# Kernel tuning notes

Measured on AMD Instinct MI355X. Metric: run time of the kernel, lower is better.

Reference implementation:

```python
import jax, jax.numpy as jnp
import numpy as np

B, S, SC, E, H = 2, 2048, 2048, 1024, 16
D = E // H
EPS = 1e-6


def _layernorm(x, g, b):
    m = jnp.mean(x, axis=-1, keepdims=True)
    v = jnp.mean((x - m) ** 2, axis=-1, keepdims=True)
    return (x - m) / jnp.sqrt(v + EPS) * g + b


def _mha(xk, xv, xq, Wk, Wv, Wq, Wo, bo, masked):
    # per-head projections, vectorized over the head axis: [B,Sx,E] x [H,E,D] -> [B,H,Sx,D]
    K = jnp.einsum('bse,hed->bhsd', xk, Wk)
    V = jnp.einsum('bse,hed->bhsd', xv, Wv)
    Q = jnp.einsum('bqe,hed->bhqd', xq, Wq)
    scores = jnp.einsum('bhqd,bhkd->bhqk', Q, K)  # [B,H,Sq,Sk]
    sk = xk.shape[1]
    if masked:
        causal = jnp.triu(jnp.ones((xq.shape[1], sk), dtype=bool), k=1)
        scores = jnp.where(causal, -jnp.inf, scores)
    att = jax.nn.softmax(scores / jnp.sqrt(jnp.asarray(sk, scores.dtype)), axis=-1)
    out = jnp.einsum('bhqk,bhkd->bhqd', att, V)
    out = out.transpose(0, 2, 1, 3).reshape(out.shape[0], out.shape[2], -1)  # concat heads -> [B,Sq,E]
    return jax.nn.relu(out @ Wo + bo)  # Dense(emb_sz, relu) output projection


def setup_inputs():
    key = jax.random.key(0)
    ks = jax.random.split(key, 16)
    w = lambda k, shape: jax.random.normal(k, shape, jnp.float32) * 0.02
    return {
        'inputs': jax.random.normal(ks[0], (B, S, E), jnp.float32),
        'context_seq': jax.random.normal(ks[1], (B, SC, E), jnp.float32),
        'Wk1': w(ks[2], (H, E, D)), 'Wv1': w(ks[3], (H, E, D)), 'Wq1': w(ks[4], (H, E, D)),
        'Wo1': w(ks[5], (E, E)), 'bo1': jnp.zeros((E,), jnp.float32),
        'Wk2': w(ks[6], (H, E, D)), 'Wv2': w(ks[7], (H, E, D)), 'Wq2': w(ks[8], (H, E, D)),
        'Wo2': w(ks[9], (E, E)), 'bo2': jnp.zeros((E,), jnp.float32),
        'Wf': w(ks[10], (E, E)), 'bf': jnp.zeros((E,), jnp.float32),
        'g1': jnp.ones((E,), jnp.float32), 'b1': jnp.zeros((E,), jnp.float32),
        'g2': jnp.ones((E,), jnp.float32), 'b2': jnp.zeros((E,), jnp.float32),
        'g3': jnp.ones((E,), jnp.float32), 'b3': jnp.zeros((E,), jnp.float32),
    }


def reference(inputs, context_seq, Wk1, Wv1, Wq1, Wo1, bo1,
              Wk2, Wv2, Wq2, Wo2, bo2, Wf, bf,
              g1, b1, g2, b2, g3, b3):
    # masked multi-head self-attention + residual + LN1 (dropout is identity at inference)
    a = _mha(inputs, inputs, inputs, Wk1, Wv1, Wq1, Wo1, bo1, masked=True)
    a = _layernorm(inputs + a, g1, b1)
    # unmasked cross-attention: K/V from context, Q from previous output
    c = _mha(context_seq, context_seq, a, Wk2, Wv2, Wq2, Wo2, bo2, masked=False)
    c = _layernorm(c + c, g2, b2)  # faithful to source: residual adds output to itself
    # FFN (single Dense(emb_sz, relu)) + residual + LN3
    f = jax.nn.relu(c @ Wf + bf)
    return _layernorm(c + f, g3, b3)
```

## Files before the change

### kernel.cpp

```cpp
#include <hip/hip_runtime.h>
#include <stdint.h>
#include <stddef.h>

typedef __bf16 bf16;
typedef __bf16 bf16x8 __attribute__((ext_vector_type(8)));
typedef __bf16 bf16x4 __attribute__((ext_vector_type(4)));
typedef float  f32x4  __attribute__((ext_vector_type(4)));
typedef uint32_t u32x4 __attribute__((ext_vector_type(4)));

#define MFMA(a, b, c) __builtin_amdgcn_mfma_f32_16x16x32_bf16((a), (b), (c), 0, 0, 0)
#define SWZE(row, chunk) (((row) << 6) + ((((chunk) ^ ((row) & 7))) << 3))

static __device__ __forceinline__ void gload_lds16(const void* g, void* l) {
  __builtin_amdgcn_global_load_lds((const __attribute__((address_space(1))) void*)g,
                                   (__attribute__((address_space(3))) void*)l,
                                   16, 0, 0);
}
static __device__ __forceinline__ void waitvm0() {
  asm volatile("s_waitcnt vmcnt(0)" ::: "memory");
}
static __device__ __forceinline__ float expq(float x) {
  float r;
  asm("v_exp_f32 %0, %1" : "=v"(r) : "v"(x));
  return r;
}
static __device__ __forceinline__ float rcpq(float x) {
  float r;
  asm("v_rcp_f32 %0, %1" : "=v"(r) : "v"(x));
  return r;
}
static __device__ __forceinline__ uint32_t cvtpk_bf16(float lo, float hi) {
  uint32_t r;
  asm("v_cvt_pk_bf16_f32 %0, %1, %2" : "=v"(r) : "v"(lo), "v"(hi));
  return r;
}
static __device__ __forceinline__ int xcd_swz(int orig, int nwg) {
  return (orig & 7) * (nwg >> 3) + (orig >> 3);
}
static __device__ __forceinline__ int vperm_store(int s) {
  return (s & ~31) | (((s >> 3) & 1) << 4) | (((s >> 2) & 1) << 3) |
         (((s >> 4) & 1) << 2) | (s & 3);
}

__global__ __launch_bounds__(256) void prep_k(
    const float* __restrict__ inp, const float* __restrict__ ctx,
    bf16* __restrict__ XB, bf16* __restrict__ CB,
    const float* __restrict__ Wq1, const float* __restrict__ Wk1,
    const float* __restrict__ Wv1, const float* __restrict__ Wq2,
    const float* __restrict__ Wk2, const float* __restrict__ Wv2,
    bf16* __restrict__ WQKV1, bf16* __restrict__ WQ2, bf16* __restrict__ WKV2,
    const float* __restrict__ Wo1, const float* __restrict__ Wo2,
    const float* __restrict__ Wf,
    bf16* __restrict__ WO1, bf16* __restrict__ WO2, bf16* __restrict__ WFt) {
  const int tid = threadIdx.x;
  int bx = blockIdx.x;
  if (bx < 8192) {
    const float* s = bx < 4096 ? inp : ctx;
    bf16* d = bx < 4096 ? XB : CB;
    size_t idx = (size_t)(bx & 4095) * 256 + tid;
    float4 v = *(const float4*)(s + idx * 4);
    bf16x4 o;
    o[0] = (bf16)v.x; o[1] = (bf16)v.y; o[2] = (bf16)v.z; o[3] = (bf16)v.w;
    *(bf16x4*)(d + idx * 4) = o;
    return;
  }
  bx -= 8192;
  __shared__ float T[64][65];
  if (bx < 1536) {
    const int wi = bx >> 8, sub = bx & 255;
    const float* src = (wi == 0) ? Wq1 : (wi == 1) ? Wk1 : (wi == 2) ? Wv1
                     : (wi == 3) ? Wq2 : (wi == 4) ? Wk2 : Wv2;
    bf16* dst = (wi == 0) ? WQKV1 : (wi == 1) ? WQKV1 + 1048576
              : (wi == 2) ? WQKV1 + 2097152 : (wi == 3) ? WQ2
              : (wi == 4) ? WKV2 : WKV2 + 1048576;
    const int e0 = (sub & 15) * 64, h = sub >> 4;
    const int er = tid >> 4, dof = (tid & 15) * 4;
#pragma unroll
    for (int i = 0; i < 4; ++i) {
      int e = i * 16 + er;
      float4 v = *(const float4*)(src + ((size_t)h * 1024 + e0 + e) * 64 + dof);
      T[e][dof] = v.x; T[e][dof + 1] = v.y; T[e][dof + 2] = v.z; T[e][dof + 3] = v.w;
    }
    __syncthreads();
    const int dr = tid >> 3, eo = (tid & 7) * 8;
#pragma unroll
    for (int i = 0; i < 2; ++i) {
      int d = i * 32 + dr;
      bf16x8 ov;
#pragma unroll
      for (int j = 0; j < 8; ++j) ov[j] = (bf16)T[eo + j][d];
      *(bf16x8*)(dst + ((size_t)h * 64 + d) * 1024 + e0 + eo) = ov;
    }
    return;
  }
  bx -= 1536;
  {
    const int wi = bx >> 8, sub = bx & 255;
    const float* src = (wi == 0) ? Wo1 : (wi == 1) ? Wo2 : Wf;
    bf16* dst = (wi == 0) ? WO1 : (wi == 1) ? WO2 : WFt;
    const int k0 = (sub & 15) * 64, n0 = (sub >> 4) * 64;
    const int kr = tid >> 4, no = (tid & 15) * 4;
#pragma unroll
    for (int i = 0; i < 4; ++i) {
      int k = i * 16 + kr;
      float4 v = *(const float4*)(src + (size_t)(k0 + k) * 1024 + n0 + no);
      T[k][no] = v.x; T[k][no + 1] = v.y; T[k][no + 2] = v.z; T[k][no + 3] = v.w;
    }
    __syncthreads();
    const int nr = tid >> 3, ko = (tid & 7) * 8;
#pragma unroll
    for (int i = 0; i < 2; ++i) {
      int n = i * 32 + nr;
      bf16x8 ov;
#pragma unroll
      for (int j = 0; j < 8; ++j) ov[j] = (bf16)T[ko + j][n];
      *(bf16x8*)(dst + (size_t)(n0 + n) * 1024 + k0 + ko) = ov;
    }
  }
}

template <int EPI>
static __device__ __forceinline__ void gemm_body(
    const bf16* __restrict__ A, const bf16* __restrict__ Bt,
    bf16* __restrict__ Cb, float* __restrict__ Cf,
    const float* __restrict__ bias, const float* __restrict__ resid,
    int N, int K, float mul, int m0, int n0, bf16* As, bf16* Bs,
    bf16* __restrict__ Vt, int colV) {
  const int tid = threadIdx.x;
  const int l = tid & 63, w = tid >> 6;
  const int l15 = l & 15, g4 = l >> 4;
  const int wr = w >> 1, wc = w & 1;
  f32x4 acc[4][4] = {};
  const int crow = tid >> 3;
  const int cko = (tid & 7) * 8;
  for (int k0 = 0; k0 < K; k0 += 64) {
#pragma unroll
    for (int i = 0; i < 4; ++i) {
      int row = i * 32 + crow;
      gload_lds16(A + (size_t)(m0 + row) * K + (k0 + cko), (char*)As + (i * 256 + tid) * 16);
      gload_lds16(Bt + (size_t)(n0 + row) * K + (k0 + cko), (char*)Bs + (i * 256 + tid) * 16);
    }
    __syncthreads();
#pragma unroll
    for (int kk = 0; kk < 2; ++kk) {
      bf16x8 af[4], bfr[4];
#pragma unroll
      for (int x = 0; x < 4; ++x) {
        af[x]  = *(const bf16x8*)&As[(wr * 64 + x * 16 + l15) * 64 + kk * 32 + g4 * 8];
        bfr[x] = *(const bf16x8*)&Bs[(wc * 64 + x * 16 + l15) * 64 + kk * 32 + g4 * 8];
      }
      __builtin_amdgcn_s_setprio(1);
#pragma unroll
      for (int mf = 0; mf < 4; ++mf)
#pragma unroll
        for (int nf = 0; nf < 4; ++nf)
          acc[mf][nf] = MFMA(af[mf], bfr[nf], acc[mf][nf]);
      __builtin_amdgcn_s_setprio(0);
    }
    __syncthreads();
  }
  if (EPI == 2 && n0 >= colV) {
#pragma unroll
    for (int mf = 0; mf < 4; ++mf)
#pragma unroll
      for (int nf = 0; nf < 4; ++nf) {
        int colrel = n0 + wc * 64 + nf * 16 + l15 - colV;
        int h = colrel >> 6, d = colrel & 63;
        int row = m0 + wr * 64 + mf * 16 + g4 * 4;
        int b = row >> 11, s = row & 2047;
        bf16x4 pv;
#pragma unroll
        for (int r = 0; r < 4; ++r) pv[r] = (bf16)acc[mf][nf][r];
        *(bf16x4*)(Vt + (((size_t)(b * 16 + h) * 64 + d) * 2048 + vperm_store(s))) = pv;
      }
    return;
  }
#pragma unroll
  for (int mf = 0; mf < 4; ++mf)
#pragma unroll
    for (int nf = 0; nf < 4; ++nf)
#pragma unroll
      for (int r = 0; r < 4; ++r) {
        int row = m0 + wr * 64 + mf * 16 + g4 * 4 + r;
        int col = n0 + wc * 64 + nf * 16 + l15;
        size_t idx = (size_t)row * N + col;
        float v = acc[mf][nf][r];
        if (EPI == 1) {
          v = mul * fmaxf(v + bias[col], 0.f);
          if (resid) v += resid[idx];
          Cf[idx] = v;
        } else {
          Cb[idx] = (bf16)v;
        }
      }
}

__global__ __launch_bounds__(256) void gemm_qkv_k(
    const bf16* __restrict__ A, const bf16* __restrict__ Bt,
    bf16* __restrict__ Cb, bf16* __restrict__ Vt, int N, int K, int colV) {
  __shared__ __align__(16) bf16 As[128 * 64];
  __shared__ __align__(16) bf16 Bs[128 * 64];
  int swz = xcd_swz(blockIdx.y * gridDim.x + blockIdx.x, gridDim.x * gridDim.y);
  int bx = swz % gridDim.x, by = swz / gridDim.x;
  gemm_body<2>(A, Bt, Cb, nullptr, nullptr, nullptr, N, K, 1.f,
               by * 128, bx * 128, As, Bs, Vt, colV);
}

__global__ __launch_bounds__(256) void gemm_bt2_k(
    const bf16* __restrict__ A0, const bf16* __restrict__ Bt0, bf16* __restrict__ C0,
    const bf16* __restrict__ A1, const bf16* __restrict__ Bt1, bf16* __restrict__ C1,
    bf16* __restrict__ Vt, int K) {
  __shared__ __align__(16) bf16 As[128 * 64];
  __shared__ __align__(16) bf16 Bs[128 * 64];
  int swz = xcd_swz(blockIdx.y * gridDim.x + blockIdx.x, gridDim.x * gridDim.y);
  int bx = swz % gridDim.x, by = swz / gridDim.x;
  if (bx < 8)
    gemm_body<0>(A0, Bt0, C0, nullptr, nullptr, nullptr, 1024, K, 1.f,
                 by * 128, bx * 128, As, Bs, nullptr, 1 << 30);
  else
    gemm_body<2>(A1, Bt1, C1, nullptr, nullptr, nullptr, 2048, K, 1.f,
                 by * 128, (bx - 8) * 128, As, Bs, Vt, 1024);
}

template <int EPI>
__global__ __launch_bounds__(512) void gemm64_k(
    const bf16* __restrict__ A, const bf16* __restrict__ Bt,
    bf16* __restrict__ Cb, float* __restrict__ Cf,
    const float* __restrict__ bias, const float* __restrict__ resid,
    int N, int K, float mul) {
  __shared__ __align__(16) bf16 As[64 * 64];
  __shared__ __align__(16) bf16 Bs[128 * 64];
  const int tid = threadIdx.x;
  const int l = tid & 63, w = tid >> 6;
  const int l15 = l & 15, g4 = l >> 4;
  const int wr = w >> 2, wc = w & 3;
  int swz = xcd_swz(blockIdx.y * gridDim.x + blockIdx.x, gridDim.x * gridDim.y);
  const int m0 = (swz / gridDim.x) * 64, n0 = (swz % gridDim.x) * 128;
  f32x4 acc[2][2] = {};
  const int crow = tid >> 3, cko = (tid & 7) * 8;
  for (int k0 = 0; k0 < K; k0 += 64) {
    gload_lds16(A + (size_t)(m0 + crow) * K + (k0 + cko), (char*)As + tid * 16);
#pragma unroll
    for (int i = 0; i < 2; ++i) {
      int row = i * 64 + crow;
      gload_lds16(Bt + (size_t)(n0 + row) * K + (k0 + cko), (char*)Bs + (i * 512 + tid) * 16);
    }
    __syncthreads();
#pragma unroll
    for (int kk = 0; kk < 2; ++kk) {
      bf16x8 af[2], bfr[2];
#pragma unroll
      for (int x = 0; x < 2; ++x) {
        af[x]  = *(const bf16x8*)&As[(wr * 32 + x * 16 + l15) * 64 + kk * 32 + g4 * 8];
        bfr[x] = *(const bf16x8*)&Bs[(wc * 32 + x * 16 + l15) * 64 + kk * 32 + g4 * 8];
      }
      __builtin_amdgcn_s_setprio(1);
#pragma unroll
      for (int mf = 0; mf < 2; ++mf)
#pragma unroll
        for (int nf = 0; nf < 2; ++nf)
          acc[mf][nf] = MFMA(af[mf], bfr[nf], acc[mf][nf]);
      __builtin_amdgcn_s_setprio(0);
    }
    __syncthreads();
  }
#pragma unroll
  for (int mf = 0; mf < 2; ++mf)
#pragma unroll
    for (int nf = 0; nf < 2; ++nf)
#pragma unroll
      for (int r = 0; r < 4; ++r) {
        int row = m0 + wr * 32 + mf * 16 + g4 * 4 + r;
        int col = n0 + wc * 32 + nf * 16 + l15;
        size_t idx = (size_t)row * N + col;
        float v = acc[mf][nf][r];
        if (EPI == 0) {
          Cb[idx] = (bf16)v;
        } else {
          v = mul * fmaxf(v + bias[col], 0.f);
          if (resid) v += resid[idx];
          Cf[idx] = v;
        }
      }
}

template <int CAUSAL>
__global__ __launch_bounds__(256) void attn_k(
    const bf16* __restrict__ Q, int ldq, size_t sBq,
    const bf16* __restrict__ Kp, int ldk, size_t sBk,
    const bf16* __restrict__ Vt,
    bf16* __restrict__ O, int ldo, size_t sBo,
    int Sk) {
  __shared__ __align__(16) char smem[32768];
  bf16* const KsBase = (bf16*)smem;
  bf16* const VsBase = (bf16*)(smem + 16384);
  const int tid = threadIdx.x;
  const int l = tid & 63, w = tid >> 6;
  const int l15 = l & 15, g4 = l >> 4;
  const int qh = w >> 1, kh = w & 1;
  const int orig = blockIdx.y * gridDim.x + blockIdx.x;
  int qt, bh;
  if (CAUSAL) {
    const int slot = orig >> 8, s = orig & 255;
    const int pb = s & 31;
    qt = (slot & 1) ? (31 - pb) : pb;
    bh = (s >> 5) * 4 + slot;
  } else {
    const int swz = xcd_swz(orig, gridDim.x * gridDim.y);
    qt = swz % gridDim.x;
    bh = swz / gridDim.x;
  }
  const int b = bh >> 4, h = bh & 15;
  const int nT = Sk >> 6;
  const int total = CAUSAL ? (qt + 1) : nT;
  const int q0b = qt * 64;
  const bf16* Qb = Q + (size_t)b * sBq + h * 64;
  const bf16* Kb = Kp + (size_t)b * sBk + h * 64;
  const bf16* Vb = Vt + ((size_t)bh * 64) * Sk;
  bf16* Ob = O + (size_t)b * sBo + h * 64;
  const float sc2 = rsqrtf((float)Sk) * 1.442695040888963f;

  bf16x8 qf[2][2];
#pragma unroll
  for (int qg = 0; qg < 2; ++qg)
#pragma unroll
    for (int kk = 0; kk < 2; ++kk) {
      bf16x8 t8 = *(const bf16x8*)(Qb + (size_t)(q0b + qh * 32 + qg * 16 + l15) * ldq +
                                   kk * 32 + g4 * 8);
#pragma unroll
      for (int j = 0; j < 8; ++j) t8[j] = (bf16)((float)t8[j] * sc2);
      qf[qg][kk] = t8;
    }

  bf16x8 onesb;
#pragma unroll
  for (int j = 0; j < 8; ++j) onesb[j] = (bf16)1.0f;

  f32x4 o[2][4] = {};
  f32x4 ol[2] = {};

  const int srow = tid >> 3, sj = tid & 7;
  auto stage = [&](int ch, int bufi) {
#pragma unroll
    for (int ii = 0; ii < 2; ++ii) {
      int row = ii * 32 + srow;
      int je = ((sj ^ (row & 7)) << 3);
      gload_lds16(Kb + (size_t)(ch * 64 + row) * ldk + je,
                  (char*)(KsBase + bufi * 4096) + (ii * 256 + tid) * 16);
      gload_lds16(Vb + (size_t)row * Sk + ch * 64 + je,
                  (char*)(VsBase + bufi * 4096) + (ii * 256 + tid) * 16);
    }
  };

  stage(0, 0);
  waitvm0();
  __builtin_amdgcn_s_barrier();

  int cur = 0;

  for (int i = 0; i < total; ++i) {
    if (i + 1 < total) stage(i + 1, cur ^ 1);

    const int k0 = i * 64;
    const bf16* ks = KsBase + cur * 4096;
    const bf16* vs = VsBase + cur * 4096;

    f32x4 s[2][2] = {};
    __builtin_amdgcn_s_setprio(1);
#pragma unroll
    for (int ksub = 0; ksub < 2; ++ksub)
#pragma unroll
      for (int kk = 0; kk < 2; ++kk) {
        bf16x8 kf = *(const bf16x8*)&ks[SWZE(kh * 32 + ksub * 16 + l15, kk * 4 + g4)];
        s[ksub][0] = MFMA(kf, qf[0][kk], s[ksub][0]);
        s[ksub][1] = MFMA(kf, qf[1][kk], s[ksub][1]);
      }
    __builtin_amdgcn_s_setprio(0);

    if (CAUSAL && i == total - 1) {
#pragma unroll
      for (int ksub = 0; ksub < 2; ++ksub)
#pragma unroll
        for (int qg = 0; qg < 2; ++qg)
#pragma unroll
          for (int r = 0; r < 4; ++r)
            if ((k0 + kh * 32 + ksub * 16 + g4 * 4 + r) > (q0b + qh * 32 + qg * 16 + l15))
              s[ksub][qg][r] = -3e38f;
    }

#pragma unroll
    for (int ksub = 0; ksub < 2; ++ksub)
#pragma unroll
      for (int qg = 0; qg < 2; ++qg) {
        s[ksub][qg][0] = expq(s[ksub][qg][0]);
        s[ksub][qg][1] = expq(s[ksub][qg][1]);
        s[ksub][qg][2] = expq(s[ksub][qg][2]);
        s[ksub][qg][3] = expq(s[ksub][qg][3]);
      }

    bf16x8 vf[4];
#pragma unroll
    for (int nf2 = 0; nf2 < 4; ++nf2)
      vf[nf2] = *(const bf16x8*)&vs[SWZE(nf2 * 16 + l15, kh * 4 + g4)];

    __builtin_amdgcn_s_setprio(1);
#pragma unroll
    for (int qg = 0; qg < 2; ++qg) {
      u32x4 td;
      td[0] = cvtpk_bf16(s[0][qg][0], s[0][qg][1]);
      td[1] = cvtpk_bf16(s[0][qg][2], s[0][qg][3]);
      td[2] = cvtpk_bf16(s[1][qg][0], s[1][qg][1]);
      td[3] = cvtpk_bf16(s[1][qg][2], s[1][qg][3]);
      bf16x8 pa = __builtin_bit_cast(bf16x8, td);
#pragma unroll
      for (int nf2 = 0; nf2 < 4; ++nf2)
        o[qg][nf2] = MFMA(pa, vf[nf2], o[qg][nf2]);
      ol[qg] = MFMA(pa, onesb, ol[qg]);
    }
    __builtin_amdgcn_s_setprio(0);

    waitvm0();
    __builtin_amdgcn_s_barrier();
    cur ^= 1;
  }

  {
    float* sc = (float*)smem;
    float* my = sc + (size_t)(qh * 64 + l) * 41;
    if (kh == 1) {
#pragma unroll
      for (int qg = 0; qg < 2; ++qg) {
#pragma unroll
        for (int nf2 = 0; nf2 < 4; ++nf2)
#pragma unroll
          for (int r = 0; r < 4; ++r) my[(qg * 4 + nf2) * 4 + r] = o[qg][nf2][r];
#pragma unroll
        for (int r = 0; r < 4; ++r) my[32 + qg * 4 + r] = ol[qg][r];
      }
    }
    __syncthreads();
    if (kh == 0) {
#pragma unroll
      for (int qg = 0; qg < 2; ++qg) {
        f32x4 lsum;
#pragma unroll
        for (int r = 0; r < 4; ++r) lsum[r] = ol[qg][r] + my[32 + qg * 4 + r];
        float inv[4];
#pragma unroll
        for (int r = 0; r < 4; ++r) inv[r] = rcpq(lsum[r]);
#pragma unroll
        for (int nf2 = 0; nf2 < 4; ++nf2)
#pragma unroll
          for (int r = 0; r < 4; ++r) {
            float v = (o[qg][nf2][r] + my[(qg * 4 + nf2) * 4 + r]) * inv[r];
            Ob[(size_t)(q0b + qh * 32 + qg * 16 + g4 * 4 + r) * ldo + nf2 * 16 + l15] = (bf16)v;
          }
      }
    }
  }
}

__global__ __launch_bounds__(256) void ln_k(const float* __restrict__ X,
                                            const float* __restrict__ g,
                                            const float* __restrict__ bta,
                                            bf16* __restrict__ outb,
                                            float* __restrict__ outf) {
  const int tid = threadIdx.x;
  const size_t row = blockIdx.x;
  const float* x = X + row * 1024;
  float4 v = *(const float4*)(x + tid * 4);
  float sum = v.x + v.y + v.z + v.w;
  float sq = v.x * v.x + v.y * v.y + v.z * v.z + v.w * v.w;
#pragma unroll
  for (int m = 1; m < 64; m <<= 1) {
    sum += __shfl_xor(sum, m);
    sq += __shfl_xor(sq, m);
  }
  __shared__ float s1[4], s2[4];
  int w = tid >> 6;
  if ((tid & 63) == 0) { s1[w] = sum; s2[w] = sq; }
  __syncthreads();
  sum = s1[0] + s1[1] + s1[2] + s1[3];
  sq = s2[0] + s2[1] + s2[2] + s2[3];
  float mean = sum * (1.f / 1024.f);
  float var = sq * (1.f / 1024.f) - mean * mean;
  float inv = rsqrtf(var + 1e-6f);
  float4 gv = *(const float4*)(g + tid * 4);
  float4 bv = *(const float4*)(bta + tid * 4);
  float y0 = (v.x - mean) * inv * gv.x + bv.x;
  float y1 = (v.y - mean) * inv * gv.y + bv.y;
  float y2 = (v.z - mean) * inv * gv.z + bv.z;
  float y3 = (v.w - mean) * inv * gv.w + bv.w;
  if (outb) {
    bf16x4 ob;
    ob[0] = (bf16)y0; ob[1] = (bf16)y1; ob[2] = (bf16)y2; ob[3] = (bf16)y3;
    *(bf16x4*)(outb + row * 1024 + tid * 4) = ob;
  }
  if (outf) {
    float4 of;
    of.x = y0; of.y = y1; of.z = y2; of.w = y3;
    *(float4*)(outf + row * 1024 + tid * 4) = of;
  }
}

extern "C" void kernel_launch(void* const* d_in, const int* in_sizes, int n_in,
                              void* d_out, int out_size, void* d_ws, size_t ws_size,
                              hipStream_t stream) {
  (void)in_sizes; (void)n_in; (void)out_size; (void)ws_size;
  const float* inp = (const float*)d_in[0];
  const float* ctx = (const float*)d_in[1];
  const float* Wk1 = (const float*)d_in[2];
  const float* Wv1 = (const float*)d_in[3];
  const float* Wq1 = (const float*)d_in[4];
  const float* Wo1 = (const float*)d_in[5];
  const float* bo1 = (const float*)d_in[6];
  const float* Wk2 = (const float*)d_in[7];
  const float* Wv2 = (const float*)d_in[8];
  const float* Wq2 = (const float*)d_in[9];
  const float* Wo2 = (const float*)d_in[10];
  const float* bo2 = (const float*)d_in[11];
  const float* Wf = (const float*)d_in[12];
  const float* bfp = (const float*)d_in[13];
  const float* g1 = (const float*)d_in[14];
  const float* b1 = (const float*)d_in[15];
  const float* g2 = (const float*)d_in[16];
  const float* b2 = (const float*)d_in[17];
  const float* g3 = (const float*)d_in[18];
  const float* b3 = (const float*)d_in[19];
  float* out = (float*)d_out;

  char* ws = (char*)d_ws;
  size_t off = 0;
  auto alloc = [&](size_t bytes) {
    char* p = ws + off;
    off += (bytes + 255) & ~(size_t)255;
    return p;
  };
  bf16* XB = (bf16*)alloc(4096ULL * 1024 * 2);
  bf16* CB = (bf16*)alloc(4096ULL * 1024 * 2);
  bf16* WQKV1 = (bf16*)alloc(3072ULL * 1024 * 2);
  bf16* WO1 = (bf16*)alloc(1024ULL * 1024 * 2);
  bf16* WQ2 = (bf16*)alloc(1024ULL * 1024 * 2);
  bf16* WKV2 = (bf16*)alloc(2048ULL * 1024 * 2);
  bf16* WO2 = (bf16*)alloc(1024ULL * 1024 * 2);
  bf16* WFt = (bf16*)alloc(1024ULL * 1024 * 2);
  bf16* QKV1 = (bf16*)alloc(4096ULL * 3072 * 2);
  bf16* V1T = (bf16*)alloc(32ULL * 64 * 2048 * 2);
  bf16* ATT1 = (bf16*)alloc(4096ULL * 1024 * 2);
  float* T1 = (float*)alloc(4096ULL * 1024 * 4);
  float* CF = (float*)alloc(4096ULL * 1024 * 4);

  bf16* AB = XB;
  bf16* CBf = CB;
  bf16* Q2 = QKV1;
  bf16* KV2 = QKV1 + 4096ULL * 1024;
  bf16* V2T = V1T;
  bf16* ATT2 = ATT1;
  float* T2 = T1;
  float* T3 = T1;

  dim3 b256(256);
  dim3 b512(512);

  prep_k<<<10496, b256, 0, stream>>>(inp, ctx, XB, CB,
                                     Wq1, Wk1, Wv1, Wq2, Wk2, Wv2,
                                     WQKV1, WQ2, WKV2,
                                     Wo1, Wo2, Wf, WO1, WO2, WFt);

  gemm_qkv_k<<<dim3(24, 32), b256, 0, stream>>>(XB, WQKV1, QKV1, V1T, 3072, 1024, 2048);
  attn_k<1><<<dim3(32, 32), b256, 0, stream>>>(QKV1, 3072, (size_t)2048 * 3072,
                                               QKV1 + 1024, 3072, (size_t)2048 * 3072,
                                               V1T, ATT1, 1024, (size_t)2048 * 1024, 2048);
  gemm64_k<1><<<dim3(8, 64), b512, 0, stream>>>(ATT1, WO1, nullptr, T1, bo1, inp,
                                                1024, 1024, 1.f);
  ln_k<<<4096, b256, 0, stream>>>(T1, g1, b1, AB, nullptr);

  gemm_bt2_k<<<dim3(24, 32), b256, 0, stream>>>(AB, WQ2, Q2, CB, WKV2, KV2, V2T, 1024);
  attn_k<0><<<dim3(32, 32), b256, 0, stream>>>(Q2, 1024, (size_t)2048 * 1024,
                                               KV2, 2048, (size_t)2048 * 2048,
                                               V2T, ATT2, 1024, (size_t)2048 * 1024, 2048);
  gemm64_k<1><<<dim3(8, 64), b512, 0, stream>>>(ATT2, WO2, nullptr, T2, bo2, nullptr,
                                                1024, 1024, 2.f);
  ln_k<<<4096, b256, 0, stream>>>(T2, g2, b2, CBf, CF);

  gemm64_k<1><<<dim3(8, 64), b512, 0, stream>>>(CBf, WFt, nullptr, T3, bfp, CF,
                                                1024, 1024, 1.f);
  ln_k<<<4096, b256, 0, stream>>>(T3, g3, b3, nullptr, out);
}
```

Before: 264.4 us.

## Double attention query tile to 128 rows with 512-thread blocks

The attention kernel now uses 512 threads (8 waves) per block and covers a 128-row query tile instead of 64, so each staged K/V chunk is shared by twice as many query rows. Staging now needs one 16-byte load per thread instead of two, the causal block remap and masking cover the last two chunks, and the grid shrinks to 16x32 blocks. The cross-wave reduction at the end is split per query group with an extra barrier to fit in shared memory. In exchange there are fewer blocks for the causal load balance, more waves per block sharing register limits, and extra barriers in the epilogue.

```diff
diff --git a/kernel.cpp b/kernel.cpp
--- a/kernel.cpp
+++ b/kernel.cpp
@@ -285,7 +285,7 @@
 }
 
 template <int CAUSAL>
-__global__ __launch_bounds__(256) void attn_k(
+__global__ __launch_bounds__(512) void attn_k(
     const bf16* __restrict__ Q, int ldq, size_t sBq,
     const bf16* __restrict__ Kp, int ldk, size_t sBk,
     const bf16* __restrict__ Vt,
@@ -302,9 +302,9 @@
   int qt, bh;
   if (CAUSAL) {
     const int slot = orig >> 8, s = orig & 255;
-    const int pb = s & 31;
-    qt = (slot & 1) ? (31 - pb) : pb;
-    bh = (s >> 5) * 4 + slot;
+    const int pb = s & 15;
+    qt = slot ? (15 - pb) : pb;
+    bh = (s >> 4) * 2 + slot;
   } else {
     const int swz = xcd_swz(orig, gridDim.x * gridDim.y);
     qt = swz % gridDim.x;
@@ -312,8 +312,9 @@
   }
   const int b = bh >> 4, h = bh & 15;
   const int nT = Sk >> 6;
-  const int total = CAUSAL ? (qt + 1) : nT;
-  const int q0b = qt * 64;
+  const int total = CAUSAL ? (2 * qt + 2) : nT;
+  const int q0b = qt * 128;
+  const int qw = q0b + qh * 32;
   const bf16* Qb = Q + (size_t)b * sBq + h * 64;
   const bf16* Kb = Kp + (size_t)b * sBk + h * 64;
   const bf16* Vb = Vt + ((size_t)bh * 64) * Sk;
@@ -325,8 +326,7 @@
   for (int qg = 0; qg < 2; ++qg)
 #pragma unroll
     for (int kk = 0; kk < 2; ++kk) {
-      bf16x8 t8 = *(const bf16x8*)(Qb + (size_t)(q0b + qh * 32 + qg * 16 + l15) * ldq +
-                                   kk * 32 + g4 * 8);
+      bf16x8 t8 = *(const bf16x8*)(Qb + (size_t)(qw + qg * 16 + l15) * ldq + kk * 32 + g4 * 8);
 #pragma unroll
       for (int j = 0; j < 8; ++j) t8[j] = (bf16)((float)t8[j] * sc2);
       qf[qg][kk] = t8;
@@ -340,16 +340,12 @@
   f32x4 ol[2] = {};
 
   const int srow = tid >> 3, sj = tid & 7;
+  const int je = ((sj ^ (srow & 7)) << 3);
   auto stage = [&](int ch, int bufi) {
-#pragma unroll
-    for (int ii = 0; ii < 2; ++ii) {
-      int row = ii * 32 + srow;
-      int je = ((sj ^ (row & 7)) << 3);
-      gload_lds16(Kb + (size_t)(ch * 64 + row) * ldk + je,
-                  (char*)(KsBase + bufi * 4096) + (ii * 256 + tid) * 16);
-      gload_lds16(Vb + (size_t)row * Sk + ch * 64 + je,
-                  (char*)(VsBase + bufi * 4096) + (ii * 256 + tid) * 16);
-    }
+    gload_lds16(Kb + (size_t)(ch * 64 + srow) * ldk + je,
+                (char*)(KsBase + bufi * 4096) + tid * 16);
+    gload_lds16(Vb + (size_t)srow * Sk + ch * 64 + je,
+                (char*)(VsBase + bufi * 4096) + tid * 16);
   };
 
   stage(0, 0);
@@ -377,14 +373,14 @@
       }
     __builtin_amdgcn_s_setprio(0);
 
-    if (CAUSAL && i == total - 1) {
+    if (CAUSAL && i >= total - 2) {
 #pragma unroll
       for (int ksub = 0; ksub < 2; ++ksub)
 #pragma unroll
         for (int qg = 0; qg < 2; ++qg)
 #pragma unroll
           for (int r = 0; r < 4; ++r)
-            if ((k0 + kh * 32 + ksub * 16 + g4 * 4 + r) > (q0b + qh * 32 + qg * 16 + l15))
+            if ((k0 + kh * 32 + ksub * 16 + g4 * 4 + r) > (qw + qg * 16 + l15))
               s[ksub][qg][r] = -3e38f;
     }
 
@@ -426,34 +422,29 @@
 
   {
     float* sc = (float*)smem;
-    float* my = sc + (size_t)(qh * 64 + l) * 41;
-    if (kh == 1) {
-#pragma unroll
-      for (int qg = 0; qg < 2; ++qg) {
+    float* my = sc + (size_t)(qh * 64 + l) * 21;
+#pragma unroll
+    for (int qg = 0; qg < 2; ++qg) {
+      __syncthreads();
+      if (kh == 1) {
 #pragma unroll
         for (int nf2 = 0; nf2 < 4; ++nf2)
 #pragma unroll
-          for (int r = 0; r < 4; ++r) my[(qg * 4 + nf2) * 4 + r] = o[qg][nf2][r];
-#pragma unroll
-        for (int r = 0; r < 4; ++r) my[32 + qg * 4 + r] = ol[qg][r];
-      }
-    }
-    __syncthreads();
-    if (kh == 0) {
-#pragma unroll
-      for (int qg = 0; qg < 2; ++qg) {
-        f32x4 lsum;
-#pragma unroll
-        for (int r = 0; r < 4; ++r) lsum[r] = ol[qg][r] + my[32 + qg * 4 + r];
+          for (int r = 0; r < 4; ++r) my[nf2 * 4 + r] = o[qg][nf2][r];
+#pragma unroll
+        for (int r = 0; r < 4; ++r) my[16 + r] = ol[qg][r];
+      }
+      __syncthreads();
+      if (kh == 0) {
         float inv[4];
 #pragma unroll
-        for (int r = 0; r < 4; ++r) inv[r] = rcpq(lsum[r]);
+        for (int r = 0; r < 4; ++r) inv[r] = rcpq(ol[qg][r] + my[16 + r]);
 #pragma unroll
         for (int nf2 = 0; nf2 < 4; ++nf2)
 #pragma unroll
           for (int r = 0; r < 4; ++r) {
-            float v = (o[qg][nf2][r] + my[(qg * 4 + nf2) * 4 + r]) * inv[r];
-            Ob[(size_t)(q0b + qh * 32 + qg * 16 + g4 * 4 + r) * ldo + nf2 * 16 + l15] = (bf16)v;
+            float v = (o[qg][nf2][r] + my[nf2 * 4 + r]) * inv[r];
+            Ob[(size_t)(qw + qg * 16 + g4 * 4 + r) * ldo + nf2 * 16 + l15] = (bf16)v;
           }
       }
     }
@@ -568,7 +559,7 @@
                                      Wo1, Wo2, Wf, WO1, WO2, WFt);
 
   gemm_qkv_k<<<dim3(24, 32), b256, 0, stream>>>(XB, WQKV1, QKV1, V1T, 3072, 1024, 2048);
-  attn_k<1><<<dim3(32, 32), b256, 0, stream>>>(QKV1, 3072, (size_t)2048 * 3072,
+  attn_k<1><<<dim3(16, 32), b512, 0, stream>>>(QKV1, 3072, (size_t)2048 * 3072,
                                                QKV1 + 1024, 3072, (size_t)2048 * 3072,
                                                V1T, ATT1, 1024, (size_t)2048 * 1024, 2048);
   gemm64_k<1><<<dim3(8, 64), b512, 0, stream>>>(ATT1, WO1, nullptr, T1, bo1, inp,
@@ -576,7 +567,7 @@
   ln_k<<<4096, b256, 0, stream>>>(T1, g1, b1, AB, nullptr);
 
   gemm_bt2_k<<<dim3(24, 32), b256, 0, stream>>>(AB, WQ2, Q2, CB, WKV2, KV2, V2T, 1024);
-  attn_k<0><<<dim3(32, 32), b256, 0, stream>>>(Q2, 1024, (size_t)2048 * 1024,
+  attn_k<0><<<dim3(16, 32), b512, 0, stream>>>(Q2, 1024, (size_t)2048 * 1024,
                                                KV2, 2048, (size_t)2048 * 2048,
                                                V2T, ATT2, 1024, (size_t)2048 * 1024, 2048);
   gemm64_k<1><<<dim3(8, 64), b512, 0, stream>>>(ATT2, WO2, nullptr, T2, bo2, nullptr,
```

Result: faster. 246.5 us (-6.8%).
